# Optimization experiments

Measured on AMD Instinct MI355X. Metric: run time of the kernel, lower is better.

Reference implementation:

```python
import jax, jax.numpy as jnp
import numpy as np

# Dimensions: B batch, NAP/NUE node counts (= permutation_size1/2), DEG fixed degree,
# EAP/EUE edge counts, D1/D2 feature dims, OUT output_dim, S sample_size.
B, NAP, NUE, DEG = 64, 256, 128, 32
EAP, EUE = NAP * DEG, NUE * DEG
D1, D2, OUT, S = 64, 32, 64, 10
LOG2PI = float(np.log(2.0 * np.pi))


def setup_inputs() -> dict:
    ks = jax.random.split(jax.random.key(0), 16)

    def u(k, shape, fan):  # torch init: uniform(-sqrt(3/fan), sqrt(3/fan))
        ini = float(np.sqrt(3.0 / fan))
        return jax.random.uniform(k, shape, jnp.float32, -ini, ini)

    return {
        "A_AP": jax.random.normal(ks[0], (B, D1, NAP), jnp.float32),
        "A_UE": jax.random.normal(ks[1], (B, D1, NUE), jnp.float32),
        "H": jax.random.normal(ks[2], (B, D2, NAP, NUE), jnp.float32),
        "Q1_AP": u(ks[3], (2 * OUT, D1), OUT * 2 * D1),
        "Q2_AP": u(ks[4], (2 * OUT, D1), OUT * 2 * D1),
        "Q1_UE": u(ks[5], (2 * OUT, D1), OUT * 2 * D1),
        "Q2_UE": u(ks[6], (2 * OUT, D1), OUT * 2 * D1),
        "P1_AP": u(ks[7], (2 * OUT, D2), OUT * 2 * D2),
        "P1_UE": u(ks[8], (2 * OUT, D2), OUT * 2 * D2),
        "Att_AP": u(ks[9], (2 * D1, 1), D1 * 2),
        "Att_UE": u(ks[10], (2 * D1, 1), D1 * 2),
        "bn_weight": jnp.ones((2 * OUT,), jnp.float32),
        "bn_bias": jnp.zeros((2 * OUT,), jnp.float32),
        "Graph_AP_reshape": jax.random.randint(ks[11], (B, 2, EAP), 0, NAP),
        "Graph_UE_reshape": jax.random.randint(ks[12], (B, 2, EUE), 0, NUE),
        "GFA_AP": jax.random.randint(ks[13], (B, NAP, DEG), 0, EAP),
        "GFA_UE": jax.random.randint(ks[14], (B, NUE, DEG), 0, EUE),
        "permutation_size1": NAP,
        "permutation_size2": NUE,
        "BATCH_SIZE": B,
    }


def _gather_nodes(A, idx):
    # A: [B, D, N], idx: [B, E] -> [B, E, D]  (replaces the outer-product+diagonal trick)
    return jnp.take_along_axis(A, idx[:, None, :], axis=2).transpose(0, 2, 1)


def _neighbor_sampling(x_i, x_j, att, key):
    # x_i, x_j: [B, E, D]; att: [2D, 1]
    score = jnp.squeeze(jnp.concatenate([x_i, x_j], axis=-1) @ att, -1)  # [B, E]
    alpha = jnp.clip(jax.nn.sigmoid(jax.nn.leaky_relu(score, 0.2)), 0.01, 0.99)
    logits = jnp.log(alpha) - jnp.log1p(-alpha)
    noise = jax.random.logistic(key, alpha.shape, alpha.dtype)
    gate = jax.nn.sigmoid((logits + noise) / 0.1)  # RelaxedBernoulli(temp=0.1).rsample()
    return x_j * gate[..., None], alpha


def _agg_edges(edge_x, gfa):
    # edge_x: [B, E, D]; gfa: [B, N, deg] indices into E -> [B, D, N] (sum over deg)
    b, n, deg = gfa.shape
    g = jnp.take_along_axis(edge_x, gfa.reshape(b, n * deg, 1), axis=1)
    return g.reshape(b, n, deg, -1).sum(2).transpose(0, 2, 1)


def _kl_bern(a, p=0.5):
    # KL(Bernoulli(a) || Bernoulli(p)) summed over edges -> [B]
    return (a * (jnp.log(a) - jnp.log(p)) + (1 - a) * (jnp.log1p(-a) - jnp.log(1 - p))).sum(-1)


def _batchnorm(x, w, b, eps=1e-5):
    # BatchNorm1d (training-mode batch stats) on [B, C, N]
    m = x.mean(axis=(0, 2), keepdims=True)
    v = jnp.mean((x - m) ** 2, axis=(0, 2), keepdims=True)
    return (x - m) / jnp.sqrt(v + eps) * w[None, :, None] + b[None, :, None]


def _info_xz(A_r, key):
    # A_r: [M, 2*OUT]; diag-Gaussian reparam, S samples, KL-ish MC estimate -> [M]
    mean, raw = A_r[:, :OUT], A_r[:, OUT:]
    std = jax.nn.softplus(raw) + 1e-10
    eps = jax.random.normal(key, (S,) + mean.shape, mean.dtype)
    Z = mean + std * eps
    logq = (-0.5 * eps ** 2 - jnp.log(std) - 0.5 * LOG2PI).sum(-1)
    logp = (-0.5 * Z ** 2 - 0.5 * LOG2PI).sum(-1)
    return (logq - logp).mean(0)


def _forward(floats, Graph_AP_reshape, Graph_UE_reshape, GFA_AP, GFA_UE, p1, p2, bs):
    (A_AP, A_UE, H, Q1_AP, Q2_AP, Q1_UE, Q2_UE,
     P1_AP, P1_UE, Att_AP, Att_UE, bn_w, bn_b) = floats
    k1, k2, k3, k4 = jax.random.split(jax.random.key(42), 4)

    xi_ap = _gather_nodes(A_AP, Graph_AP_reshape[:, 1])
    xj_ap = _gather_nodes(A_AP, Graph_AP_reshape[:, 0])
    xi_ue = _gather_nodes(A_UE, Graph_UE_reshape[:, 1])
    xj_ue = _gather_nodes(A_UE, Graph_UE_reshape[:, 0])

    xj_ap, alpha_ap = _neighbor_sampling(xi_ap, xj_ap, Att_AP, k1)
    xj_ue, alpha_ue = _neighbor_sampling(xi_ue, xj_ue, Att_UE, k2)

    Aap = _agg_edges(xj_ap, GFA_AP)  # [B, D1, NAP]
    Aue = _agg_edges(xj_ue, GFA_UE)  # [B, D1, NUE]

    I_AZ_AP = _kl_bern(alpha_ap)
    I_AZ_UE = _kl_bern(alpha_ue)

    ap = (2.0 * jnp.einsum('od,bdn->bon', Q1_AP, Aap)
          + 2.0 * jnp.einsum('od,bd->bo', Q2_AP, Aue.mean(-1))[:, :, None]
          + 0.1 * jnp.einsum('od,bdn->bon', P1_AP, H.mean(-1)))
    ue = (2.0 * jnp.einsum('od,bdn->bon', Q1_UE, Aue)
          + 2.0 * jnp.einsum('od,bd->bo', Q2_UE, Aap.mean(-1))[:, :, None]
          + 0.1 * jnp.einsum('od,bdn->bon', P1_UE, H.mean(-2)))

    ap = _batchnorm(jax.nn.relu(ap), bn_w, bn_b)
    ue = _batchnorm(jax.nn.relu(ue), bn_w, bn_b)

    I_XZ_AP = _info_xz(ap.transpose(0, 2, 1).reshape(bs * p1, 2 * OUT), k3).reshape(bs, p1).sum(-1)
    I_XZ_UE = _info_xz(ue.transpose(0, 2, 1).reshape(bs * p2, 2 * OUT), k4).reshape(bs, p2).sum(-1)

    return ap[:, :OUT], ue[:, :OUT], I_XZ_AP, I_XZ_UE, I_AZ_AP, I_AZ_UE


def reference(A_AP, A_UE, H, Q1_AP, Q2_AP, Q1_UE, Q2_UE, P1_AP, P1_UE,
              Att_AP, Att_UE, bn_weight, bn_bias,
              Graph_AP_reshape, Graph_UE_reshape, GFA_AP, GFA_UE,
              permutation_size1, permutation_size2, BATCH_SIZE):
    floats = (A_AP, A_UE, H, Q1_AP, Q2_AP, Q1_UE, Q2_UE,
              P1_AP, P1_UE, Att_AP, Att_UE, bn_weight, bn_bias)
    return _forward(floats, Graph_AP_reshape, Graph_UE_reshape, GFA_AP, GFA_UE,
                    permutation_size1, permutation_size2, BATCH_SIZE)
```

## Files before the change

### kernel.cpp

```cpp
#include <hip/hip_runtime.h>
#include <math.h>

#define BB   64
#define NAP  256
#define NUE  128
#define DEG  32
#define EAP  (NAP*DEG)
#define EUE  (NUE*DEG)
#define D1   64
#define D2   32
#define OUTC 64
#define CH   128
#define SS   10

#define TINYF 1.17549435e-38f
#define LOG_HALF (-0.69314718f)

constexpr unsigned rotl_c(unsigned v, int s) { return (v << s) | (v >> (32 - s)); }
struct KeyPair { unsigned hi, lo; };
constexpr KeyPair tf_ck(unsigned k0, unsigned k1, unsigned x0, unsigned x1) {
  unsigned ks2 = k0 ^ k1 ^ 0x1BD11BDAu;
  x0 += k0; x1 += k1;
  const int R[20] = {13,15,26,6, 17,29,16,24, 13,15,26,6, 17,29,16,24, 13,15,26,6};
  const unsigned ia[5] = {k1, ks2, k0, k1, ks2};
  const unsigned ib[5] = {ks2, k0, k1, ks2, k0};
  for (int g = 0; g < 5; ++g) {
    for (int j = 0; j < 4; ++j) { x0 += x1; x1 = rotl_c(x1, R[g*4+j]); x1 ^= x0; }
    x0 += ia[g]; x1 += ib[g] + (unsigned)(g + 1);
  }
  return KeyPair{x0, x1};
}
constexpr KeyPair SK1 = tf_ck(0u, 42u, 0u, 0u);
constexpr KeyPair SK2 = tf_ck(0u, 42u, 0u, 1u);
constexpr KeyPair SK3 = tf_ck(0u, 42u, 0u, 2u);
constexpr KeyPair SK4 = tf_ck(0u, 42u, 0u, 3u);

__device__ __forceinline__ unsigned rb32(unsigned k0, unsigned k1, unsigned ctr) {
  const unsigned ks2 = k0 ^ k1 ^ 0x1BD11BDAu;
  unsigned x0 = k0;
  unsigned x1 = ctr + k1;
#define TFR(r) { x0 += x1; x1 = (x1 << r) | (x1 >> (32 - r)); x1 ^= x0; }
  TFR(13) TFR(15) TFR(26) TFR(6)
  x0 += k1;  x1 += ks2 + 1u;
  TFR(17) TFR(29) TFR(16) TFR(24)
  x0 += ks2; x1 += k0 + 2u;
  TFR(13) TFR(15) TFR(26) TFR(6)
  x0 += k0;  x1 += k1 + 3u;
  TFR(17) TFR(29) TFR(16) TFR(24)
  x0 += k1;  x1 += ks2 + 4u;
  TFR(13) TFR(15) TFR(26) TFR(6)
  x0 += ks2; x1 += k0 + 5u;
#undef TFR
  return x0 ^ x1;
}

__device__ __forceinline__ float bits_to_unit(unsigned bits) {
  return __uint_as_float((bits >> 9) | 0x3f800000u) - 1.0f;
}

__device__ __forceinline__ float erfinv_f32(float x) {
  float w = -log1pf(-x * x);
  float p;
  if (w < 5.0f) {
    w = w - 2.5f;
    p = 2.81022636e-08f;
    p = fmaf(p, w, 3.43273939e-07f);
    p = fmaf(p, w, -3.5233877e-06f);
    p = fmaf(p, w, -4.39150654e-06f);
    p = fmaf(p, w, 0.00021858087f);
    p = fmaf(p, w, -0.00125372503f);
    p = fmaf(p, w, -0.00417768164f);
    p = fmaf(p, w, 0.246640727f);
    p = fmaf(p, w, 1.50140941f);
  } else {
    w = sqrtf(w) - 3.0f;
    p = -0.000200214257f;
    p = fmaf(p, w, 0.000100950558f);
    p = fmaf(p, w, 0.00134934322f);
    p = fmaf(p, w, -0.00367342844f);
    p = fmaf(p, w, 0.00573950773f);
    p = fmaf(p, w, -0.0076224613f);
    p = fmaf(p, w, 0.00943887047f);
    p = fmaf(p, w, 1.00167406f);
    p = fmaf(p, w, 2.83297682f);
  }
  return p * x;
}

__device__ __forceinline__ float normal_from_bits(unsigned bits) {
  float f = bits_to_unit(bits);
  const float lo = -0.99999994f;
  float u = fmaxf(lo, fmaf(f, 2.0f, lo));
  return 1.41421354f * erfinv_f32(u);
}

__device__ __forceinline__ float softplus_f(float x) {
  return fmaxf(x, 0.0f) + log1pf(expf(-fabsf(x)));
}

__global__ __launch_bounds__(256) void edge_kernel(
    const float* __restrict__ A_AP, const float* __restrict__ A_UE,
    const int* __restrict__ GAP, const int* __restrict__ GUE,
    const float* __restrict__ AttAP, const float* __restrict__ AttUE,
    float* __restrict__ gAP, float* __restrict__ gUE,
    float* __restrict__ IAZ_AP, float* __restrict__ IAZ_UE,
    float* __restrict__ amAP, float* __restrict__ amUE)
{
  const int side = blockIdx.y;
  const int b = blockIdx.x;
  const int N = side ? NUE : NAP;
  const int E = side ? EUE : EAP;
  const float* A  = (side ? A_UE : A_AP) + (size_t)b * D1 * N;
  const int* G    = (side ? GUE : GAP) + (size_t)b * 2 * E;
  const float* At = side ? AttUE : AttAP;
  float* gate     = (side ? gUE : gAP) + (size_t)b * E;
  float* IAZ      = side ? IAZ_UE : IAZ_AP;
  float* am       = side ? amUE : amAP;
  const unsigned k0 = side ? SK2.hi : SK1.hi;
  const unsigned k1 = side ? SK2.lo : SK1.lo;
  const int t = threadIdx.x;

  if (t < D1) am[b * D1 + t] = 0.f;

  __shared__ float si_s[NAP];
  __shared__ float sj_s[NAP];
  if (t < N) {
    float a0 = 0.f, a1 = 0.f;
    #pragma unroll
    for (int d = 0; d < D1; ++d) {
      float v = A[d * N + t];
      a0 = fmaf(v, At[d], a0);
      a1 = fmaf(v, At[D1 + d], a1);
    }
    si_s[t] = a0; sj_s[t] = a1;
  }
  __syncthreads();

  float klacc = 0.f;
  for (int e = t; e < E; e += 256) {
    const int ii = G[E + e];
    const int jj = G[e];
    float score = si_s[ii] + sj_s[jj];
    float l = (score >= 0.f) ? score : 0.2f * score;
    float sig = 1.f / (1.f + expf(-l));
    float a = fminf(fmaxf(sig, 0.01f), 0.99f);
    float logits = logf(a) - log1pf(-a);
    unsigned bits = rb32(k0, k1, (unsigned)(b * E + e));
    float f = bits_to_unit(bits);
    float u = fmaxf(TINYF, f + TINYF);
    float noise = logf(u) - log1pf(-u);
    float gv = 1.f / (1.f + expf(-((logits + noise) / 0.1f)));
    gate[e] = gv;
    klacc += a * (logf(a) - LOG_HALF) + (1.f - a) * (log1pf(-a) - LOG_HALF);
  }
  #pragma unroll
  for (int m = 32; m; m >>= 1) klacc += __shfl_xor(klacc, m, 64);
  __shared__ float red[4];
  if ((t & 63) == 0) red[t >> 6] = klacc;
  __syncthreads();
  if (t == 0) IAZ[b] = red[0] + red[1] + red[2] + red[3];
}

__global__ __launch_bounds__(256) void agg_kernel(
    const float* __restrict__ A_AP, const float* __restrict__ A_UE,
    const int* __restrict__ GAP, const int* __restrict__ GUE,
    const float* __restrict__ gAP, const float* __restrict__ gUE,
    const int* __restrict__ GFA_AP, const int* __restrict__ GFA_UE,
    float* __restrict__ Aap, float* __restrict__ Aue,
    float* __restrict__ amAP, float* __restrict__ amUE)
{
  __shared__ float Als[D1 * NAP];
  const int x = blockIdx.x;
  const int side = (x >= NAP / 64);
  const int tile = side ? x - NAP / 64 : x;
  const int b = blockIdx.y;
  const int N = side ? NUE : NAP;
  const int E = side ? EUE : EAP;
  const float* A  = (side ? A_UE : A_AP) + (size_t)b * D1 * N;
  const int* G0   = (side ? GUE : GAP) + (size_t)b * 2 * E;
  const float* gb = (side ? gUE : gAP) + (size_t)b * E;
  float* Aout = side ? Aue : Aap;
  float* am   = side ? amUE : amAP;

  const int t = threadIdx.x;
  const int wave = t >> 6, lane = t & 63;
  const int n = tile * 64 + lane;

  const int* gfa = (side ? GFA_UE : GFA_AP) + ((size_t)b * N + n) * DEG;
  int jj[DEG]; float gg[DEG];
  #pragma unroll
  for (int k = 0; k < DEG; ++k) {
    int e = gfa[k];
    jj[k] = G0[e];
    gg[k] = gb[e];
  }

  for (int idx = t * 4; idx < D1 * N; idx += 1024)
    *(float4*)(Als + idx) = *(const float4*)(A + idx);
  __syncthreads();

  for (int dd = 0; dd < 16; ++dd) {
    const int d = wave * 16 + dd;
    const float* Ar = Als + d * N;
    float acc = 0.f;
    #pragma unroll
    for (int k = 0; k < DEG; ++k) acc = fmaf(gg[k], Ar[jj[k]], acc);
    Aout[((size_t)b * D1 + d) * N + n] = acc;
    float s = acc;
    #pragma unroll
    for (int m = 32; m; m >>= 1) s += __shfl_xor(s, m, 64);
    if (lane == 0) atomicAdd(&am[b * D1 + d], s);
  }
}

__global__ __launch_bounds__(256) void hreduce_kernel(
    const float* __restrict__ H, float* __restrict__ Hm1, float* __restrict__ Hm2)
{
  const int bd = blockIdx.x;
  const float* Hp = H + (size_t)bd * NAP * NUE;
  const int t = threadIdx.x;
  const int tx = t & 31, ty = t >> 5;
  float4 col = {0.f, 0.f, 0.f, 0.f};
  #pragma unroll 4
  for (int i = ty; i < NAP; i += 8) {
    float4 v = ((const float4*)(Hp + (size_t)i * NUE))[tx];
    col.x += v.x; col.y += v.y; col.z += v.z; col.w += v.w;
    float rs = v.x + v.y + v.z + v.w;
    #pragma unroll
    for (int m = 16; m; m >>= 1) rs += __shfl_xor(rs, m, 64);
    if (tx == 0) Hm1[(size_t)bd * NAP + i] = rs * (1.0f / NUE);
  }
  __shared__ float cp[8 * 128];
  ((float4*)cp)[ty * 32 + tx] = col;
  __syncthreads();
  if (t < 128) {
    float s = 0.f;
    #pragma unroll
    for (int r = 0; r < 8; ++r) s += cp[r * 128 + t];
    Hm2[(size_t)bd * NUE + t] = s * (1.0f / NAP);
  }
}

__global__ __launch_bounds__(128) void qterm_kernel(
    const float* __restrict__ Q2_AP, const float* __restrict__ Q2_UE,
    const float* __restrict__ AapMeanRaw, const float* __restrict__ AueMeanRaw,
    float* __restrict__ qbAP, float* __restrict__ qbUE,
    float* __restrict__ stAP, float* __restrict__ stUE)
{
  const int b = blockIdx.x;
  const int o = threadIdx.x;
  if (b == 0) {
    #pragma unroll
    for (int i = o; i < 2 * CH; i += 128) { stAP[i] = 0.f; stUE[i] = 0.f; }
  }
  float sA = 0.f, sU = 0.f;
  #pragma unroll
  for (int d = 0; d < D1; ++d) {
    float mUE = AueMeanRaw[b * D1 + d] * (1.0f / NUE);
    float mAP = AapMeanRaw[b * D1 + d] * (1.0f / NAP);
    sA = fmaf(Q2_AP[o * D1 + d], mUE, sA);
    sU = fmaf(Q2_UE[o * D1 + d], mAP, sU);
  }
  qbAP[b * CH + o] = 2.f * sA;
  qbUE[b * CH + o] = 2.f * sU;
}

__global__ __launch_bounds__(256) void mix_kernel(
    const float* __restrict__ Aap, const float* __restrict__ Aue,
    const float* __restrict__ Hm1, const float* __restrict__ Hm2,
    const float* __restrict__ Q1_AP, const float* __restrict__ Q1_UE,
    const float* __restrict__ P1_AP, const float* __restrict__ P1_UE,
    const float* __restrict__ qbAP, const float* __restrict__ qbUE,
    float* __restrict__ preAP, float* __restrict__ preUE,
    float* __restrict__ stAP, float* __restrict__ stUE)
{
  __shared__ float Qs[CH * 65];
  __shared__ float Ps[CH * 33];
  __shared__ float As[D1 * 64];
  __shared__ float Hs[D2 * 64];
  const int x = blockIdx.x;
  const int side = (x >= NAP / 64);
  const int tile = side ? x - NAP / 64 : x;
  const int b = blockIdx.y;
  const int N = side ? NUE : NAP;
  const float* Aagg = (side ? Aue : Aap) + (size_t)b * D1 * N + tile * 64;
  const float* Hm   = (side ? Hm2 : Hm1) + (size_t)b * D2 * N + tile * 64;
  const float* Q1   = side ? Q1_UE : Q1_AP;
  const float* P1   = side ? P1_UE : P1_AP;
  const float* qb   = (side ? qbUE : qbAP) + b * CH;
  float* pre        = (side ? preUE : preAP) + (size_t)b * CH * N + tile * 64;
  float* stat       = side ? stUE : stAP;

  const int t = threadIdx.x;
  for (int i = t; i < CH * D1; i += 256) Qs[(i >> 6) * 65 + (i & 63)] = Q1[i];
  for (int i = t; i < CH * D2; i += 256) Ps[(i >> 5) * 33 + (i & 31)] = P1[i];
  for (int i = t; i < D1 * 64; i += 256) As[i] = Aagg[(size_t)(i >> 6) * N + (i & 63)];
  for (int i = t; i < D2 * 64; i += 256) Hs[i] = Hm[(size_t)(i >> 6) * N + (i & 63)];
  __syncthreads();

  const int tn = t & 15, to = t >> 4;
  float accQ[8][4] = {};
  for (int d = 0; d < D1; ++d) {
    float4 a = *(const float4*)&As[d * 64 + tn * 4];
    #pragma unroll
    for (int oi = 0; oi < 8; ++oi) {
      float w = Qs[(to * 8 + oi) * 65 + d];
      accQ[oi][0] = fmaf(w, a.x, accQ[oi][0]);
      accQ[oi][1] = fmaf(w, a.y, accQ[oi][1]);
      accQ[oi][2] = fmaf(w, a.z, accQ[oi][2]);
      accQ[oi][3] = fmaf(w, a.w, accQ[oi][3]);
    }
  }
  float accP[8][4] = {};
  for (int c = 0; c < D2; ++c) {
    float4 h = *(const float4*)&Hs[c * 64 + tn * 4];
    #pragma unroll
    for (int oi = 0; oi < 8; ++oi) {
      float w = Ps[(to * 8 + oi) * 33 + c];
      accP[oi][0] = fmaf(w, h.x, accP[oi][0]);
      accP[oi][1] = fmaf(w, h.y, accP[oi][1]);
      accP[oi][2] = fmaf(w, h.z, accP[oi][2]);
      accP[oi][3] = fmaf(w, h.w, accP[oi][3]);
    }
  }
  #pragma unroll
  for (int oi = 0; oi < 8; ++oi) {
    const int o = to * 8 + oi;
    const float base = qb[o];
    float4 r;
    r.x = fmaxf(2.f * accQ[oi][0] + base + 0.1f * accP[oi][0], 0.f);
    r.y = fmaxf(2.f * accQ[oi][1] + base + 0.1f * accP[oi][1], 0.f);
    r.z = fmaxf(2.f * accQ[oi][2] + base + 0.1f * accP[oi][2], 0.f);
    r.w = fmaxf(2.f * accQ[oi][3] + base + 0.1f * accP[oi][3], 0.f);
    *(float4*)&pre[(size_t)o * N + tn * 4] = r;
    float s1 = r.x + r.y + r.z + r.w;
    float s2 = r.x * r.x + r.y * r.y + r.z * r.z + r.w * r.w;
    #pragma unroll
    for (int m = 1; m < 16; m <<= 1) { s1 += __shfl_xor(s1, m, 64); s2 += __shfl_xor(s2, m, 64); }
    if (tn == 0) { atomicAdd(&stat[o], s1); atomicAdd(&stat[CH + o], s2); }
  }
}

__global__ __launch_bounds__(256) void bnfinal_kernel(
    const float* __restrict__ statAP, const float* __restrict__ statUE,
    const float* __restrict__ bnw, const float* __restrict__ bnb,
    float* __restrict__ ssAP, float* __restrict__ ssUE,
    float* __restrict__ IXZ)
{
  const int t = threadIdx.x;
  if (t < 2 * BB) IXZ[t] = 0.f;
  if (t < CH) {
    const float inv = 1.0f / (BB * NAP);
    float m = statAP[t] * inv;
    float v = statAP[CH + t] * inv - m * m;
    float sc = bnw[t] / sqrtf(v + 1e-5f);
    ssAP[t] = sc; ssAP[CH + t] = bnb[t] - m * sc;
  } else {
    const int o = t - CH;
    const float inv = 1.0f / (BB * NUE);
    float m = statUE[o] * inv;
    float v = statUE[CH + o] * inv - m * m;
    float sc = bnw[o] / sqrtf(v + 1e-5f);
    ssUE[o] = sc; ssUE[CH + o] = bnb[o] - m * sc;
  }
}

__global__ __launch_bounds__(256) void finalize_kernel(
    const float* __restrict__ preAP, const float* __restrict__ preUE,
    const float* __restrict__ ssAP, const float* __restrict__ ssUE,
    float* __restrict__ outAP, float* __restrict__ outUE,
    float* __restrict__ IXZAP, float* __restrict__ IXZUE)
{
  const int side = blockIdx.z;
  const int N = side ? NUE : NAP;
  if ((int)blockIdx.x * 64 >= N) return;
  const float* pre = side ? preUE : preAP;
  const float* ss  = side ? ssUE  : ssAP;
  float* outp      = side ? outUE : outAP;
  float* IXZ       = side ? IXZUE : IXZAP;
  const unsigned k0 = side ? SK4.hi : SK3.hi;
  const unsigned k1 = side ? SK4.lo : SK3.lo;
  const int ROWS = BB * N;

  const int b = blockIdx.y;
  const int lane = threadIdx.x & 63;
  const int og = threadIdx.x >> 6;
  const int n = blockIdx.x * 64 + lane;
  const int row = b * N + n;
  const float* preb = pre + (size_t)b * CH * N;

  float accZ = 0.f, sumlog = 0.f;
  for (int oi = 0; oi < 16; ++oi) {
    const int o = og * 16 + oi;
    float mpre = preb[o * N + n];
    float rraw = preb[(o + 64) * N + n];
    float x0 = fmaf(mpre, ss[o], ss[CH + o]);
    float x1 = fmaf(rraw, ss[o + 64], ss[CH + o + 64]);
    outp[((size_t)b * OUTC + o) * N + n] = x0;
    float stdv = softplus_f(x1) + 1e-10f;
    sumlog += logf(stdv);
    #pragma unroll
    for (int s = 0; s < SS; ++s) {
      unsigned idx = (unsigned)((s * ROWS + row) * 64 + o);
      float eps = normal_from_bits(rb32(k0, k1, idx));
      float Z = fmaf(stdv, eps, x0);
      accZ += 0.5f * (Z * Z - eps * eps);
    }
  }
  __shared__ float pz[4][64];
  __shared__ float pl[4][64];
  pz[og][lane] = accZ; pl[og][lane] = sumlog;
  __syncthreads();
  if (og == 0) {
    float az = pz[0][lane] + pz[1][lane] + pz[2][lane] + pz[3][lane];
    float al = pl[0][lane] + pl[1][lane] + pl[2][lane] + pl[3][lane];
    float rv = az * (1.0f / SS) - al;
    #pragma unroll
    for (int m = 32; m; m >>= 1) rv += __shfl_xor(rv, m, 64);
    if (lane == 0) atomicAdd(&IXZ[b], rv);
  }
}

constexpr size_t OFF_AMEAN_AP = 0;
constexpr size_t OFF_AMEAN_UE = OFF_AMEAN_AP + BB * D1;
constexpr size_t OFF_STAT_AP  = OFF_AMEAN_UE + BB * D1;
constexpr size_t OFF_STAT_UE  = OFF_STAT_AP + 2 * CH;
constexpr size_t OFF_GATE_AP  = OFF_STAT_UE + 2 * CH;
constexpr size_t OFF_GATE_UE  = OFF_GATE_AP + (size_t)BB * EAP;
constexpr size_t OFF_AAP      = OFF_GATE_UE + (size_t)BB * EUE;
constexpr size_t OFF_AUE      = OFF_AAP + (size_t)BB * D1 * NAP;
constexpr size_t OFF_HM1      = OFF_AUE + (size_t)BB * D1 * NUE;
constexpr size_t OFF_HM2      = OFF_HM1 + (size_t)BB * D2 * NAP;
constexpr size_t OFF_PRE_AP   = OFF_HM2 + (size_t)BB * D2 * NUE;
constexpr size_t OFF_PRE_UE   = OFF_PRE_AP + (size_t)BB * CH * NAP;
constexpr size_t OFF_QB_AP    = OFF_PRE_UE + (size_t)BB * CH * NUE;
constexpr size_t OFF_QB_UE    = OFF_QB_AP + BB * CH;
constexpr size_t OFF_SS_AP    = OFF_QB_UE + BB * CH;
constexpr size_t OFF_SS_UE    = OFF_SS_AP + 2 * CH;
constexpr size_t WS_FLOATS    = OFF_SS_UE + 2 * CH;

extern "C" void kernel_launch(void* const* d_in, const int* in_sizes, int n_in,
                              void* d_out, int out_size, void* d_ws, size_t ws_size,
                              hipStream_t stream)
{
  const float* A_AP  = (const float*)d_in[0];
  const float* A_UE  = (const float*)d_in[1];
  const float* H     = (const float*)d_in[2];
  const float* Q1_AP = (const float*)d_in[3];
  const float* Q2_AP = (const float*)d_in[4];
  const float* Q1_UE = (const float*)d_in[5];
  const float* Q2_UE = (const float*)d_in[6];
  const float* P1_AP = (const float*)d_in[7];
  const float* P1_UE = (const float*)d_in[8];
  const float* AttAP = (const float*)d_in[9];
  const float* AttUE = (const float*)d_in[10];
  const float* bnw   = (const float*)d_in[11];
  const float* bnb   = (const float*)d_in[12];
  const int* GraphAP = (const int*)d_in[13];
  const int* GraphUE = (const int*)d_in[14];
  const int* GFA_AP  = (const int*)d_in[15];
  const int* GFA_UE  = (const int*)d_in[16];

  float* ws = (float*)d_ws;
  if (ws_size < WS_FLOATS * sizeof(float)) return;

  float* amAP  = ws + OFF_AMEAN_AP;
  float* amUE  = ws + OFF_AMEAN_UE;
  float* stAP  = ws + OFF_STAT_AP;
  float* stUE  = ws + OFF_STAT_UE;
  float* gAP   = ws + OFF_GATE_AP;
  float* gUE   = ws + OFF_GATE_UE;
  float* Aap   = ws + OFF_AAP;
  float* Aue   = ws + OFF_AUE;
  float* Hm1   = ws + OFF_HM1;
  float* Hm2   = ws + OFF_HM2;
  float* preAP = ws + OFF_PRE_AP;
  float* preUE = ws + OFF_PRE_UE;
  float* qbAP  = ws + OFF_QB_AP;
  float* qbUE  = ws + OFF_QB_UE;
  float* ssAP  = ws + OFF_SS_AP;
  float* ssUE  = ws + OFF_SS_UE;

  float* out     = (float*)d_out;
  float* outAP   = out;
  float* outUE   = out + (size_t)BB * OUTC * NAP;
  float* IXZ_AP  = out + (size_t)BB * OUTC * (NAP + NUE);
  float* IXZ_UE  = IXZ_AP + BB;
  float* IAZ_AP  = IXZ_UE + BB;
  float* IAZ_UE  = IAZ_AP + BB;

  edge_kernel<<<dim3(BB, 2), 256, 0, stream>>>(
      A_AP, A_UE, GraphAP, GraphUE, AttAP, AttUE,
      gAP, gUE, IAZ_AP, IAZ_UE, amAP, amUE);

  hreduce_kernel<<<BB * D2, 256, 0, stream>>>(H, Hm1, Hm2);

  agg_kernel<<<dim3(NAP / 64 + NUE / 64, BB), 256, 0, stream>>>(
      A_AP, A_UE, GraphAP, GraphUE, gAP, gUE, GFA_AP, GFA_UE,
      Aap, Aue, amAP, amUE);

  qterm_kernel<<<BB, 128, 0, stream>>>(Q2_AP, Q2_UE, amAP, amUE, qbAP, qbUE, stAP, stUE);

  mix_kernel<<<dim3(NAP / 64 + NUE / 64, BB), 256, 0, stream>>>(
      Aap, Aue, Hm1, Hm2, Q1_AP, Q1_UE, P1_AP, P1_UE,
      qbAP, qbUE, preAP, preUE, stAP, stUE);

  bnfinal_kernel<<<1, 256, 0, stream>>>(stAP, stUE, bnw, bnb, ssAP, ssUE, IXZ_AP);

  finalize_kernel<<<dim3(NAP / 64, BB, 2), 256, 0, stream>>>(
      preAP, preUE, ssAP, ssUE, outAP, outUE, IXZ_AP, IXZ_UE);
}
```

Measured before the change: 669.1 us.

## Fuse edge, aggregation, H-reduce, qterm and bnfinal into fewer kernels

Merges edge gating, neighbour aggregation and the H reduction into one kernel with one block per (batch, side) plus H-reduce blocks. Gates are recomputed per node from the GFA lists, so the gate buffer is never written to or read from global memory. The q-bias is folded into mix_kernel and the batch-norm scale/shift into finalize_kernel, cutting seven launches to three. The cost is much less parallelism for aggregation: 128 blocks, each doing all rows serially with only N threads active and staging A in halves through shared memory. Gates are also computed redundantly per incident edge.

```diff
diff --git a/kernel.cpp b/kernel.cpp
--- a/kernel.cpp
+++ b/kernel.cpp
@@ -12,6 +12,7 @@
 #define OUTC 64
 #define CH   128
 #define SS   10
+#define NEB  (BB*2)
 
 #define TINYF 1.17549435e-38f
 #define LOG_HALF (-0.69314718f)
@@ -98,125 +99,21 @@
   return fmaxf(x, 0.0f) + log1pf(expf(-fabsf(x)));
 }
 
-__global__ __launch_bounds__(256) void edge_kernel(
-    const float* __restrict__ A_AP, const float* __restrict__ A_UE,
-    const int* __restrict__ GAP, const int* __restrict__ GUE,
-    const float* __restrict__ AttAP, const float* __restrict__ AttUE,
-    float* __restrict__ gAP, float* __restrict__ gUE,
-    float* __restrict__ IAZ_AP, float* __restrict__ IAZ_UE,
-    float* __restrict__ amAP, float* __restrict__ amUE)
-{
-  const int side = blockIdx.y;
-  const int b = blockIdx.x;
-  const int N = side ? NUE : NAP;
-  const int E = side ? EUE : EAP;
-  const float* A  = (side ? A_UE : A_AP) + (size_t)b * D1 * N;
-  const int* G    = (side ? GUE : GAP) + (size_t)b * 2 * E;
-  const float* At = side ? AttUE : AttAP;
-  float* gate     = (side ? gUE : gAP) + (size_t)b * E;
-  float* IAZ      = side ? IAZ_UE : IAZ_AP;
-  float* am       = side ? amUE : amAP;
-  const unsigned k0 = side ? SK2.hi : SK1.hi;
-  const unsigned k1 = side ? SK2.lo : SK1.lo;
-  const int t = threadIdx.x;
-
-  if (t < D1) am[b * D1 + t] = 0.f;
-
-  __shared__ float si_s[NAP];
-  __shared__ float sj_s[NAP];
-  if (t < N) {
-    float a0 = 0.f, a1 = 0.f;
-    #pragma unroll
-    for (int d = 0; d < D1; ++d) {
-      float v = A[d * N + t];
-      a0 = fmaf(v, At[d], a0);
-      a1 = fmaf(v, At[D1 + d], a1);
-    }
-    si_s[t] = a0; sj_s[t] = a1;
-  }
-  __syncthreads();
-
-  float klacc = 0.f;
-  for (int e = t; e < E; e += 256) {
-    const int ii = G[E + e];
-    const int jj = G[e];
-    float score = si_s[ii] + sj_s[jj];
-    float l = (score >= 0.f) ? score : 0.2f * score;
-    float sig = 1.f / (1.f + expf(-l));
-    float a = fminf(fmaxf(sig, 0.01f), 0.99f);
-    float logits = logf(a) - log1pf(-a);
-    unsigned bits = rb32(k0, k1, (unsigned)(b * E + e));
-    float f = bits_to_unit(bits);
-    float u = fmaxf(TINYF, f + TINYF);
-    float noise = logf(u) - log1pf(-u);
-    float gv = 1.f / (1.f + expf(-((logits + noise) / 0.1f)));
-    gate[e] = gv;
-    klacc += a * (logf(a) - LOG_HALF) + (1.f - a) * (log1pf(-a) - LOG_HALF);
-  }
-  #pragma unroll
-  for (int m = 32; m; m >>= 1) klacc += __shfl_xor(klacc, m, 64);
-  __shared__ float red[4];
-  if ((t & 63) == 0) red[t >> 6] = klacc;
-  __syncthreads();
-  if (t == 0) IAZ[b] = red[0] + red[1] + red[2] + red[3];
-}
-
-__global__ __launch_bounds__(256) void agg_kernel(
-    const float* __restrict__ A_AP, const float* __restrict__ A_UE,
-    const int* __restrict__ GAP, const int* __restrict__ GUE,
-    const float* __restrict__ gAP, const float* __restrict__ gUE,
-    const int* __restrict__ GFA_AP, const int* __restrict__ GFA_UE,
-    float* __restrict__ Aap, float* __restrict__ Aue,
-    float* __restrict__ amAP, float* __restrict__ amUE)
-{
-  __shared__ float Als[D1 * NAP];
-  const int x = blockIdx.x;
-  const int side = (x >= NAP / 64);
-  const int tile = side ? x - NAP / 64 : x;
-  const int b = blockIdx.y;
-  const int N = side ? NUE : NAP;
-  const int E = side ? EUE : EAP;
-  const float* A  = (side ? A_UE : A_AP) + (size_t)b * D1 * N;
-  const int* G0   = (side ? GUE : GAP) + (size_t)b * 2 * E;
-  const float* gb = (side ? gUE : gAP) + (size_t)b * E;
-  float* Aout = side ? Aue : Aap;
-  float* am   = side ? amUE : amAP;
-
-  const int t = threadIdx.x;
-  const int wave = t >> 6, lane = t & 63;
-  const int n = tile * 64 + lane;
-
-  const int* gfa = (side ? GFA_UE : GFA_AP) + ((size_t)b * N + n) * DEG;
-  int jj[DEG]; float gg[DEG];
-  #pragma unroll
-  for (int k = 0; k < DEG; ++k) {
-    int e = gfa[k];
-    jj[k] = G0[e];
-    gg[k] = gb[e];
-  }
-
-  for (int idx = t * 4; idx < D1 * N; idx += 1024)
-    *(float4*)(Als + idx) = *(const float4*)(A + idx);
-  __syncthreads();
-
-  for (int dd = 0; dd < 16; ++dd) {
-    const int d = wave * 16 + dd;
-    const float* Ar = Als + d * N;
-    float acc = 0.f;
-    #pragma unroll
-    for (int k = 0; k < DEG; ++k) acc = fmaf(gg[k], Ar[jj[k]], acc);
-    Aout[((size_t)b * D1 + d) * N + n] = acc;
-    float s = acc;
-    #pragma unroll
-    for (int m = 32; m; m >>= 1) s += __shfl_xor(s, m, 64);
-    if (lane == 0) atomicAdd(&am[b * D1 + d], s);
-  }
-}
-
-__global__ __launch_bounds__(256) void hreduce_kernel(
+__device__ __forceinline__ float gate_of(float score, unsigned k0, unsigned k1, unsigned ctr) {
+  float l = (score >= 0.f) ? score : 0.2f * score;
+  float sig = 1.f / (1.f + expf(-l));
+  float a = fminf(fmaxf(sig, 0.01f), 0.99f);
+  float logits = logf(a) - log1pf(-a);
+  unsigned bits = rb32(k0, k1, ctr);
+  float f = bits_to_unit(bits);
+  float u = fmaxf(TINYF, f + TINYF);
+  float noise = logf(u) - log1pf(-u);
+  return 1.f / (1.f + expf(-((logits + noise) / 0.1f)));
+}
+
+__device__ __forceinline__ void hreduce_body(int bd, float* cp,
     const float* __restrict__ H, float* __restrict__ Hm1, float* __restrict__ Hm2)
 {
-  const int bd = blockIdx.x;
   const float* Hp = H + (size_t)bd * NAP * NUE;
   const int t = threadIdx.x;
   const int tx = t & 31, ty = t >> 5;
@@ -230,7 +127,6 @@
     for (int m = 16; m; m >>= 1) rs += __shfl_xor(rs, m, 64);
     if (tx == 0) Hm1[(size_t)bd * NAP + i] = rs * (1.0f / NUE);
   }
-  __shared__ float cp[8 * 128];
   ((float4*)cp)[ty * 32 + tx] = col;
   __syncthreads();
   if (t < 128) {
@@ -241,43 +137,126 @@
   }
 }
 
-__global__ __launch_bounds__(128) void qterm_kernel(
-    const float* __restrict__ Q2_AP, const float* __restrict__ Q2_UE,
-    const float* __restrict__ AapMeanRaw, const float* __restrict__ AueMeanRaw,
-    float* __restrict__ qbAP, float* __restrict__ qbUE,
-    float* __restrict__ stAP, float* __restrict__ stUE)
+__global__ __launch_bounds__(256) void k1_kernel(
+    const float* __restrict__ A_AP, const float* __restrict__ A_UE,
+    const float* __restrict__ H,
+    const int* __restrict__ GAP, const int* __restrict__ GUE,
+    const float* __restrict__ AttAP, const float* __restrict__ AttUE,
+    const int* __restrict__ GFA_AP, const int* __restrict__ GFA_UE,
+    float* __restrict__ Aap, float* __restrict__ Aue,
+    float* __restrict__ amAP, float* __restrict__ amUE,
+    float* __restrict__ Hm1, float* __restrict__ Hm2,
+    float* __restrict__ IAZ_AP, float* __restrict__ IAZ_UE,
+    float* __restrict__ stat0, float* __restrict__ IXZ0)
 {
-  const int b = blockIdx.x;
-  const int o = threadIdx.x;
-  if (b == 0) {
-    #pragma unroll
-    for (int i = o; i < 2 * CH; i += 128) { stAP[i] = 0.f; stUE[i] = 0.f; }
-  }
-  float sA = 0.f, sU = 0.f;
+  __shared__ float smem[8192 + NAP + NAP + D1];
+  __shared__ float red2[4];
+  const int x = blockIdx.x;
+  const int t = threadIdx.x;
+  if (x >= NEB) { hreduce_body(x - NEB, smem, H, Hm1, Hm2); return; }
+
+  if (x == 0) {
+    for (int i = t; i < 4 * CH; i += 256) stat0[i] = 0.f;
+    for (int i = t; i < 2 * BB; i += 256) IXZ0[i] = 0.f;
+  }
+  const int side = x & 1, b = x >> 1;
+  const int N = side ? NUE : NAP;
+  const int E = N * DEG;
+  const float* A  = (side ? A_UE : A_AP) + (size_t)b * D1 * N;
+  const int* G    = (side ? GUE : GAP) + (size_t)b * 2 * E;
+  const float* At = side ? AttUE : AttAP;
+  const int* gfa  = (side ? GFA_UE : GFA_AP) + (size_t)b * N * DEG;
+  float* Aout = (side ? Aue : Aap) + (size_t)b * D1 * N;
+  float* am   = (side ? amUE : amAP) + b * D1;
+  float* IAZ  = side ? IAZ_UE : IAZ_AP;
+  const unsigned k0 = side ? SK2.hi : SK1.hi;
+  const unsigned k1 = side ? SK2.lo : SK1.lo;
+
+  float* Als  = smem;
+  float* si_s = smem + 8192;
+  float* sj_s = si_s + NAP;
+  float* am_s = sj_s + NAP;
+
+  if (t < D1) am_s[t] = 0.f;
+  if (t < N) {
+    float a0 = 0.f, a1 = 0.f;
+    #pragma unroll
+    for (int d = 0; d < D1; ++d) {
+      float v = A[d * N + t];
+      a0 = fmaf(v, At[d], a0);
+      a1 = fmaf(v, At[D1 + d], a1);
+    }
+    si_s[t] = a0; sj_s[t] = a1;
+  }
+  __syncthreads();
+
+  float klacc = 0.f;
+  for (int e = t; e < E; e += 256) {
+    float score = si_s[G[E + e]] + sj_s[G[e]];
+    float l = (score >= 0.f) ? score : 0.2f * score;
+    float sig = 1.f / (1.f + expf(-l));
+    float a = fminf(fmaxf(sig, 0.01f), 0.99f);
+    klacc += a * (logf(a) - LOG_HALF) + (1.f - a) * (log1pf(-a) - LOG_HALF);
+  }
   #pragma unroll
-  for (int d = 0; d < D1; ++d) {
-    float mUE = AueMeanRaw[b * D1 + d] * (1.0f / NUE);
-    float mAP = AapMeanRaw[b * D1 + d] * (1.0f / NAP);
-    sA = fmaf(Q2_AP[o * D1 + d], mUE, sA);
-    sU = fmaf(Q2_UE[o * D1 + d], mAP, sU);
-  }
-  qbAP[b * CH + o] = 2.f * sA;
-  qbUE[b * CH + o] = 2.f * sU;
+  for (int m = 32; m; m >>= 1) klacc += __shfl_xor(klacc, m, 64);
+  if ((t & 63) == 0) red2[t >> 6] = klacc;
+  __syncthreads();
+  if (t == 0) IAZ[b] = red2[0] + red2[1] + red2[2] + red2[3];
+
+  int jj[DEG]; float gv[DEG];
+  if (t < N) {
+    const int* gf = gfa + t * DEG;
+    #pragma unroll
+    for (int k = 0; k < DEG; ++k) {
+      int e = gf[k];
+      int ii = G[E + e];
+      jj[k] = G[e];
+      float score = si_s[ii] + sj_s[jj[k]];
+      gv[k] = gate_of(score, k0, k1, (unsigned)(b * E + e));
+    }
+  }
+
+  const int HR = side ? D1 : 32;
+  const int halves = side ? 1 : 2;
+  for (int h = 0; h < halves; ++h) {
+    __syncthreads();
+    const float* Ah = A + (size_t)h * HR * N;
+    for (int idx = t * 4; idx < HR * N; idx += 1024)
+      *(float4*)(Als + idx) = *(const float4*)(Ah + idx);
+    __syncthreads();
+    if (t < N) {
+      for (int dr = 0; dr < HR; ++dr) {
+        const int d = h * HR + dr;
+        const float* Ar = Als + dr * N;
+        float acc = 0.f;
+        #pragma unroll
+        for (int k = 0; k < DEG; ++k) acc = fmaf(gv[k], Ar[jj[k]], acc);
+        Aout[(size_t)d * N + t] = acc;
+        float s = acc;
+        #pragma unroll
+        for (int m = 32; m; m >>= 1) s += __shfl_xor(s, m, 64);
+        if ((t & 63) == 0) atomicAdd(&am_s[d], s);
+      }
+    }
+  }
+  __syncthreads();
+  if (t < D1) am[t] = am_s[t];
 }
 
 __global__ __launch_bounds__(256) void mix_kernel(
     const float* __restrict__ Aap, const float* __restrict__ Aue,
     const float* __restrict__ Hm1, const float* __restrict__ Hm2,
     const float* __restrict__ Q1_AP, const float* __restrict__ Q1_UE,
+    const float* __restrict__ Q2_AP, const float* __restrict__ Q2_UE,
     const float* __restrict__ P1_AP, const float* __restrict__ P1_UE,
-    const float* __restrict__ qbAP, const float* __restrict__ qbUE,
+    const float* __restrict__ amAP, const float* __restrict__ amUE,
     float* __restrict__ preAP, float* __restrict__ preUE,
     float* __restrict__ stAP, float* __restrict__ stUE)
 {
-  __shared__ float Qs[CH * 65];
-  __shared__ float Ps[CH * 33];
-  __shared__ float As[D1 * 64];
-  __shared__ float Hs[D2 * 64];
+  __shared__ float qb_s[CH];
+  __shared__ float am_s[D1];
+  __shared__ float U[CH * 65 + D1 * 64];
   const int x = blockIdx.x;
   const int side = (x >= NAP / 64);
   const int tile = side ? x - NAP / 64 : x;
@@ -286,16 +265,27 @@
   const float* Aagg = (side ? Aue : Aap) + (size_t)b * D1 * N + tile * 64;
   const float* Hm   = (side ? Hm2 : Hm1) + (size_t)b * D2 * N + tile * 64;
   const float* Q1   = side ? Q1_UE : Q1_AP;
+  const float* Q2   = side ? Q2_UE : Q2_AP;
   const float* P1   = side ? P1_UE : P1_AP;
-  const float* qb   = (side ? qbUE : qbAP) + b * CH;
+  const float* amO  = side ? amAP : amUE;
+  const float invO  = side ? (1.0f / NAP) : (1.0f / NUE);
   float* pre        = (side ? preUE : preAP) + (size_t)b * CH * N + tile * 64;
   float* stat       = side ? stUE : stAP;
 
   const int t = threadIdx.x;
+  if (t < D1) am_s[t] = amO[b * D1 + t] * invO;
+  __syncthreads();
+  if (t < CH) {
+    float s = 0.f;
+    #pragma unroll
+    for (int d = 0; d < D1; ++d) s = fmaf(Q2[t * D1 + d], am_s[d], s);
+    qb_s[t] = 2.f * s;
+  }
+
+  float* Qs = U;
+  float* As = U + CH * 65;
   for (int i = t; i < CH * D1; i += 256) Qs[(i >> 6) * 65 + (i & 63)] = Q1[i];
-  for (int i = t; i < CH * D2; i += 256) Ps[(i >> 5) * 33 + (i & 31)] = P1[i];
   for (int i = t; i < D1 * 64; i += 256) As[i] = Aagg[(size_t)(i >> 6) * N + (i & 63)];
-  for (int i = t; i < D2 * 64; i += 256) Hs[i] = Hm[(size_t)(i >> 6) * N + (i & 63)];
   __syncthreads();
 
   const int tn = t & 15, to = t >> 4;
@@ -311,6 +301,14 @@
       accQ[oi][3] = fmaf(w, a.w, accQ[oi][3]);
     }
   }
+  __syncthreads();
+
+  float* Ps = U;
+  float* Hs = U + CH * 33;
+  for (int i = t; i < CH * D2; i += 256) Ps[(i >> 5) * 33 + (i & 31)] = P1[i];
+  for (int i = t; i < D2 * 64; i += 256) Hs[i] = Hm[(size_t)(i >> 6) * N + (i & 63)];
+  __syncthreads();
+
   float accP[8][4] = {};
   for (int c = 0; c < D2; ++c) {
     float4 h = *(const float4*)&Hs[c * 64 + tn * 4];
@@ -323,10 +321,11 @@
       accP[oi][3] = fmaf(w, h.w, accP[oi][3]);
     }
   }
+
   #pragma unroll
   for (int oi = 0; oi < 8; ++oi) {
     const int o = to * 8 + oi;
-    const float base = qb[o];
+    const float base = qb_s[o];
     float4 r;
     r.x = fmaxf(2.f * accQ[oi][0] + base + 0.1f * accP[oi][0], 0.f);
     r.y = fmaxf(2.f * accQ[oi][1] + base + 0.1f * accP[oi][1], 0.f);
@@ -341,51 +340,40 @@
   }
 }
 
-__global__ __launch_bounds__(256) void bnfinal_kernel(
-    const float* __restrict__ statAP, const float* __restrict__ statUE,
-    const float* __restrict__ bnw, const float* __restrict__ bnb,
-    float* __restrict__ ssAP, float* __restrict__ ssUE,
-    float* __restrict__ IXZ)
-{
-  const int t = threadIdx.x;
-  if (t < 2 * BB) IXZ[t] = 0.f;
-  if (t < CH) {
-    const float inv = 1.0f / (BB * NAP);
-    float m = statAP[t] * inv;
-    float v = statAP[CH + t] * inv - m * m;
-    float sc = bnw[t] / sqrtf(v + 1e-5f);
-    ssAP[t] = sc; ssAP[CH + t] = bnb[t] - m * sc;
-  } else {
-    const int o = t - CH;
-    const float inv = 1.0f / (BB * NUE);
-    float m = statUE[o] * inv;
-    float v = statUE[CH + o] * inv - m * m;
-    float sc = bnw[o] / sqrtf(v + 1e-5f);
-    ssUE[o] = sc; ssUE[CH + o] = bnb[o] - m * sc;
-  }
-}
-
 __global__ __launch_bounds__(256) void finalize_kernel(
     const float* __restrict__ preAP, const float* __restrict__ preUE,
-    const float* __restrict__ ssAP, const float* __restrict__ ssUE,
+    const float* __restrict__ stAP, const float* __restrict__ stUE,
+    const float* __restrict__ bnw, const float* __restrict__ bnb,
     float* __restrict__ outAP, float* __restrict__ outUE,
     float* __restrict__ IXZAP, float* __restrict__ IXZUE)
 {
-  const int side = blockIdx.z;
+  const int x = blockIdx.x;
+  const int side = (x >= NAP / 64);
+  const int tile = side ? x - NAP / 64 : x;
   const int N = side ? NUE : NAP;
-  if ((int)blockIdx.x * 64 >= N) return;
-  const float* pre = side ? preUE : preAP;
-  const float* ss  = side ? ssUE  : ssAP;
-  float* outp      = side ? outUE : outAP;
-  float* IXZ       = side ? IXZUE : IXZAP;
+  const float* pre  = side ? preUE : preAP;
+  const float* stat = side ? stUE : stAP;
+  float* outp       = side ? outUE : outAP;
+  float* IXZ        = side ? IXZUE : IXZAP;
   const unsigned k0 = side ? SK4.hi : SK3.hi;
   const unsigned k1 = side ? SK4.lo : SK3.lo;
   const int ROWS = BB * N;
+  const int t = threadIdx.x;
+
+  __shared__ float ss_s[2 * CH];
+  if (t < CH) {
+    const float inv = 1.0f / (float)ROWS;
+    float m = stat[t] * inv;
+    float v = stat[CH + t] * inv - m * m;
+    float sc = bnw[t] / sqrtf(v + 1e-5f);
+    ss_s[t] = sc; ss_s[CH + t] = bnb[t] - m * sc;
+  }
+  __syncthreads();
 
   const int b = blockIdx.y;
-  const int lane = threadIdx.x & 63;
-  const int og = threadIdx.x >> 6;
-  const int n = blockIdx.x * 64 + lane;
+  const int lane = t & 63;
+  const int og = t >> 6;
+  const int n = tile * 64 + lane;
   const int row = b * N + n;
   const float* preb = pre + (size_t)b * CH * N;
 
@@ -394,8 +382,8 @@
     const int o = og * 16 + oi;
     float mpre = preb[o * N + n];
     float rraw = preb[(o + 64) * N + n];
-    float x0 = fmaf(mpre, ss[o], ss[CH + o]);
-    float x1 = fmaf(rraw, ss[o + 64], ss[CH + o + 64]);
+    float x0 = fmaf(mpre, ss_s[o], ss_s[CH + o]);
+    float x1 = fmaf(rraw, ss_s[o + 64], ss_s[CH + o + 64]);
     outp[((size_t)b * OUTC + o) * N + n] = x0;
     float stdv = softplus_f(x1) + 1e-10f;
     sumlog += logf(stdv);
@@ -425,19 +413,13 @@
 constexpr size_t OFF_AMEAN_UE = OFF_AMEAN_AP + BB * D1;
 constexpr size_t OFF_STAT_AP  = OFF_AMEAN_UE + BB * D1;
 constexpr size_t OFF_STAT_UE  = OFF_STAT_AP + 2 * CH;
-constexpr size_t OFF_GATE_AP  = OFF_STAT_UE + 2 * CH;
-constexpr size_t OFF_GATE_UE  = OFF_GATE_AP + (size_t)BB * EAP;
-constexpr size_t OFF_AAP      = OFF_GATE_UE + (size_t)BB * EUE;
+constexpr size_t OFF_AAP      = OFF_STAT_UE + 2 * CH;
 constexpr size_t OFF_AUE      = OFF_AAP + (size_t)BB * D1 * NAP;
 constexpr size_t OFF_HM1      = OFF_AUE + (size_t)BB * D1 * NUE;
 constexpr size_t OFF_HM2      = OFF_HM1 + (size_t)BB * D2 * NAP;
 constexpr size_t OFF_PRE_AP   = OFF_HM2 + (size_t)BB * D2 * NUE;
 constexpr size_t OFF_PRE_UE   = OFF_PRE_AP + (size_t)BB * CH * NAP;
-constexpr size_t OFF_QB_AP    = OFF_PRE_UE + (size_t)BB * CH * NUE;
-constexpr size_t OFF_QB_UE    = OFF_QB_AP + BB * CH;
-constexpr size_t OFF_SS_AP    = OFF_QB_UE + BB * CH;
-constexpr size_t OFF_SS_UE    = OFF_SS_AP + 2 * CH;
-constexpr size_t WS_FLOATS    = OFF_SS_UE + 2 * CH;
+constexpr size_t WS_FLOATS    = OFF_PRE_UE + (size_t)BB * CH * NUE;
 
 extern "C" void kernel_launch(void* const* d_in, const int* in_sizes, int n_in,
                               void* d_out, int out_size, void* d_ws, size_t ws_size,
@@ -468,18 +450,12 @@
   float* amUE  = ws + OFF_AMEAN_UE;
   float* stAP  = ws + OFF_STAT_AP;
   float* stUE  = ws + OFF_STAT_UE;
-  float* gAP   = ws + OFF_GATE_AP;
-  float* gUE   = ws + OFF_GATE_UE;
   float* Aap   = ws + OFF_AAP;
   float* Aue   = ws + OFF_AUE;
   float* Hm1   = ws + OFF_HM1;
   float* Hm2   = ws + OFF_HM2;
   float* preAP = ws + OFF_PRE_AP;
   float* preUE = ws + OFF_PRE_UE;
-  float* qbAP  = ws + OFF_QB_AP;
-  float* qbUE  = ws + OFF_QB_UE;
-  float* ssAP  = ws + OFF_SS_AP;
-  float* ssUE  = ws + OFF_SS_UE;
 
   float* out     = (float*)d_out;
   float* outAP   = out;
@@ -489,24 +465,14 @@
   float* IAZ_AP  = IXZ_UE + BB;
   float* IAZ_UE  = IAZ_AP + BB;
 
-  edge_kernel<<<dim3(BB, 2), 256, 0, stream>>>(
-      A_AP, A_UE, GraphAP, GraphUE, AttAP, AttUE,
-      gAP, gUE, IAZ_AP, IAZ_UE, amAP, amUE);
-
-  hreduce_kernel<<<BB * D2, 256, 0, stream>>>(H, Hm1, Hm2);
-
-  agg_kernel<<<dim3(NAP / 64 + NUE / 64, BB), 256, 0, stream>>>(
-      A_AP, A_UE, GraphAP, GraphUE, gAP, gUE, GFA_AP, GFA_UE,
-      Aap, Aue, amAP, amUE);
-
-  qterm_kernel<<<BB, 128, 0, stream>>>(Q2_AP, Q2_UE, amAP, amUE, qbAP, qbUE, stAP, stUE);
+  k1_kernel<<<dim3(NEB + BB * D2), 256, 0, stream>>>(
+      A_AP, A_UE, H, GraphAP, GraphUE, AttAP, AttUE, GFA_AP, GFA_UE,
+      Aap, Aue, amAP, amUE, Hm1, Hm2, IAZ_AP, IAZ_UE, stAP, IXZ_AP);
 
   mix_kernel<<<dim3(NAP / 64 + NUE / 64, BB), 256, 0, stream>>>(
-      Aap, Aue, Hm1, Hm2, Q1_AP, Q1_UE, P1_AP, P1_UE,
-      qbAP, qbUE, preAP, preUE, stAP, stUE);
-
-  bnfinal_kernel<<<1, 256, 0, stream>>>(stAP, stUE, bnw, bnb, ssAP, ssUE, IXZ_AP);
-
-  finalize_kernel<<<dim3(NAP / 64, BB, 2), 256, 0, stream>>>(
-      preAP, preUE, ssAP, ssUE, outAP, outUE, IXZ_AP, IXZ_UE);
-}
+      Aap, Aue, Hm1, Hm2, Q1_AP, Q1_UE, Q2_AP, Q2_UE, P1_AP, P1_UE,
+      amAP, amUE, preAP, preUE, stAP, stUE);
+
+  finalize_kernel<<<dim3(NAP / 64 + NUE / 64, BB), 256, 0, stream>>>(
+      preAP, preUE, stAP, stUE, bnw, bnb, outAP, outUE, IXZ_AP, IXZ_UE);
+}
```

New measurement: 645.5 us. 1.04x faster.
